# Kernel tuning notes

Measured on AMD Instinct MI355X. Metric: run time of the kernel, lower is better.

Reference implementation:

```python
import jax, jax.numpy as jnp
import numpy as np

N = 100000   # nodes
E = 1600000  # edges (no self loops; module adds them)
D = 128      # in_dim == out_dim
BN_EPS = 1e-5
NORM_EPS = 1e-12


def setup_inputs() -> dict:
    key = jax.random.key(0)
    ks = jax.random.split(key, 9)
    x = jax.random.normal(ks[0], (N, D), jnp.float32)
    src = jax.random.randint(ks[1], (E,), 0, N, dtype=jnp.int32)
    dst = jax.random.randint(ks[2], (E,), 0, N, dtype=jnp.int32)
    dst = jnp.where(dst == src, (dst + 1) % N, dst)  # no pre-existing self loops
    edge_index = jnp.stack([src, dst], axis=0)
    edge_w = jax.random.uniform(ks[3], (E, 2), jnp.float32)
    # MySAGEConv.linear: Linear(2*D -> D) since concat=True
    W_lin = jax.random.normal(ks[4], (2 * D, D), jnp.float32) * (1.0 / np.sqrt(2 * D))
    b_lin = jnp.zeros((D,), jnp.float32)
    # BatchNorm1d(D)
    gamma = jnp.ones((D,), jnp.float32)
    beta = jnp.zeros((D,), jnp.float32)
    # PositionEmbedding(2, D): Linear(2->D//2, no bias), ReLU, Linear(D//2->D, no bias)
    pos_w1 = jax.random.normal(ks[5], (2, D // 2), jnp.float32) * 0.1
    pos_w2 = jax.random.normal(ks[6], (D // 2, D), jnp.float32) * 0.1
    return {"x": x, "edge_index": edge_index, "edge_w": edge_w,
            "W_lin": W_lin, "b_lin": b_lin, "gamma": gamma, "beta": beta,
            "pos_w1": pos_w1, "pos_w2": pos_w2}


def reference(x, edge_index, edge_w, W_lin, b_lin, gamma, beta, pos_w1, pos_w2):
    src, dst = edge_index[0], edge_index[1]
    # Position embedding is computed by the block but DISCARDED inside MySAGEConv.forward,
    # because add_remaining_self_loops(edge_index, None, 1, N) overwrites edge_weight with None.
    _pe = jnp.maximum(edge_w @ pos_w1, 0.0) @ pos_w2  # [E, D], unused (faithful to bug)
    # add_remaining_self_loops: append a self loop for every node
    loops = jnp.arange(N, dtype=src.dtype)
    src_f = jnp.concatenate([src, loops])
    dst_f = jnp.concatenate([dst, loops])
    # message = x_j (edge_weight is None); aggr = 'mean' scatter over destinations
    msg = x[src_f]                                           # [E+N, D] gather
    summed = jax.ops.segment_sum(msg, dst_f, num_segments=N)  # [N, D] scatter-add
    cnt = jax.ops.segment_sum(jnp.ones((E + N, 1), x.dtype), dst_f, num_segments=N)
    aggr = summed / cnt                                      # every node has >=1 (self loop)
    # update: concat + linear + L2 normalize
    h = jnp.concatenate([x, aggr], axis=-1) @ W_lin + b_lin   # [N, D]
    h = h / jnp.maximum(jnp.linalg.norm(h, axis=-1, keepdims=True), NORM_EPS)
    # BatchNorm1d (training-mode batch stats, biased variance)
    mu = jnp.mean(h, axis=0)
    var = jnp.var(h, axis=0)
    h = (h - mu) * jax.lax.rsqrt(var + BN_EPS) * gamma + beta
    # residual (in_dim == out_dim) + ReLU
    return jnp.maximum(h + x, 0.0)
```

## Files before the change

kernel.cpp:

```cpp
#include <hip/hip_runtime.h>
#include <hip/hip_bf16.h>

typedef __attribute__((ext_vector_type(4))) float f32x4;
typedef __attribute__((ext_vector_type(8))) short short8;
typedef unsigned short u16;
typedef unsigned long long u64;

#define NSLICE 64
#define LDSN 12544

static __device__ __forceinline__ u16 f2bf(float f) {
    __hip_bfloat16 h = __float2bfloat16(f);
    return __builtin_bit_cast(u16, h);
}
static __device__ __forceinline__ float bf2f(u16 u) {
    unsigned int w = ((unsigned int)u) << 16;
    return __builtin_bit_cast(float, w);
}

__global__ void k_pre(const float* __restrict__ x, u16* __restrict__ xb, int total8,
                      const int* __restrict__ dst, int* __restrict__ part,
                      int E, int chunk, int n, int cvtBlocks, int sl4) {
    __shared__ int lh[LDSN];
    int tid = threadIdx.x;
    if ((int)blockIdx.x < cvtBlocks) {
        const float4* x4 = (const float4*)x;
        int stride = cvtBlocks * 256;
        for (int i = blockIdx.x * 256 + tid; i < total8; i += stride) {
            float4 a = x4[i * 2], b = x4[i * 2 + 1];
            union { u16 u[8]; short8 v; } o;
            o.u[0] = f2bf(a.x); o.u[1] = f2bf(a.y); o.u[2] = f2bf(a.z); o.u[3] = f2bf(a.w);
            o.u[4] = f2bf(b.x); o.u[5] = f2bf(b.y); o.u[6] = f2bf(b.z); o.u[7] = f2bf(b.w);
            *(short8*)(xb + (size_t)i * 8) = o.v;
        }
    } else {
        int b = blockIdx.x - cvtBlocks;
        int g = b & 7;
        int s = b >> 3;
        int lo = g * chunk;
        int hi = min(lo + chunk, n);
        int cnt = hi - lo;
        for (int i = tid; i < cnt; i += 256) lh[i] = 0;
        __syncthreads();
        int E4 = E >> 2;
        const int4* d4 = (const int4*)dst;
        int i40 = s * sl4, i41 = min(i40 + sl4, E4);
        for (int i = i40 + tid; i < i41; i += 256) {
            int4 v = d4[i];
            if (v.x >= lo && v.x < hi) atomicAdd(&lh[v.x - lo], 1);
            if (v.y >= lo && v.y < hi) atomicAdd(&lh[v.y - lo], 1);
            if (v.z >= lo && v.z < hi) atomicAdd(&lh[v.z - lo], 1);
            if (v.w >= lo && v.w < hi) atomicAdd(&lh[v.w - lo], 1);
        }
        if (s == NSLICE - 1) {
            for (int e = E4 * 4 + tid; e < E; e += 256) {
                int d = dst[e];
                if (d >= lo && d < hi) atomicAdd(&lh[d - lo], 1);
            }
        }
        __syncthreads();
        int* pp = part + (size_t)s * n + lo;
        for (int i = tid; i < cnt; i += 256) pp[i] = lh[i];
    }
}

__global__ void k_scan_a(int* __restrict__ part, int* __restrict__ deg,
                         int* __restrict__ bsum, int n) {
    __shared__ int sm[256];
    int tid = threadIdx.x;
    int i = blockIdx.x * 256 + tid;
    int tot = 0;
    if (i < n) {
        int run = 0;
#pragma unroll
        for (int s = 0; s < NSLICE; ++s) {
            size_t idx = (size_t)s * n + i;
            int t = part[idx];
            part[idx] = run;
            run += t;
        }
        tot = run;
        deg[i] = run;
    }
    sm[tid] = tot;
    __syncthreads();
    for (int ofs = 128; ofs > 0; ofs >>= 1) {
        if (tid < ofs) sm[tid] += sm[tid + ofs];
        __syncthreads();
    }
    if (tid == 0) bsum[blockIdx.x] = sm[0];
}

__global__ void k_scan_b(const int* __restrict__ bsum, int* __restrict__ boff, int nb,
                         int* __restrict__ offN) {
    __shared__ int s[512];
    int tid = threadIdx.x;
    int v = (tid < nb) ? bsum[tid] : 0;
    s[tid] = v;
    __syncthreads();
    for (int ofs = 1; ofs < 512; ofs <<= 1) {
        int t = (tid >= ofs) ? s[tid - ofs] : 0;
        __syncthreads();
        s[tid] += t;
        __syncthreads();
    }
    if (tid < nb) boff[tid] = s[tid] - v;
    if (tid == nb - 1) offN[0] = s[tid];
}

__global__ void k_scan_c(const int* __restrict__ deg, const int* __restrict__ boff,
                         int* __restrict__ off, int n) {
    __shared__ int s[256];
    int tid = threadIdx.x;
    int i = blockIdx.x * 256 + tid;
    int v = (i < n) ? deg[i] : 0;
    s[tid] = v;
    __syncthreads();
    for (int ofs = 1; ofs < 256; ofs <<= 1) {
        int t = (tid >= ofs) ? s[tid - ofs] : 0;
        __syncthreads();
        s[tid] += t;
        __syncthreads();
    }
    int excl = s[tid] - v + boff[blockIdx.x];
    if (i < n) off[i] = excl;
}

__global__ void k_fill(const int* __restrict__ src, const int* __restrict__ dst,
                       const int* __restrict__ off, const int* __restrict__ pre,
                       int* __restrict__ csr, int E, int chunk, int n, int sl4) {
    __shared__ int lcnt[LDSN];
    int tid = threadIdx.x;
    int g = blockIdx.x & 7;
    int s = blockIdx.x >> 3;
    int lo = g * chunk;
    int hi = min(lo + chunk, n);
    int cnt = hi - lo;
    for (int i = tid; i < cnt; i += 256) lcnt[i] = 0;
    __syncthreads();
    int E4 = E >> 2;
    const int4* d4 = (const int4*)dst;
    const int4* s4 = (const int4*)src;
    const int* prs = pre + (size_t)s * n;
    int i40 = s * sl4, i41 = min(i40 + sl4, E4);
    for (int i = i40 + tid; i < i41; i += 256) {
        int4 v = d4[i];
        int4 u = s4[i];
        if (v.x >= lo && v.x < hi) {
            int p = off[v.x] + prs[v.x] + atomicAdd(&lcnt[v.x - lo], 1);
            csr[p] = u.x;
        }
        if (v.y >= lo && v.y < hi) {
            int p = off[v.y] + prs[v.y] + atomicAdd(&lcnt[v.y - lo], 1);
            csr[p] = u.y;
        }
        if (v.z >= lo && v.z < hi) {
            int p = off[v.z] + prs[v.z] + atomicAdd(&lcnt[v.z - lo], 1);
            csr[p] = u.z;
        }
        if (v.w >= lo && v.w < hi) {
            int p = off[v.w] + prs[v.w] + atomicAdd(&lcnt[v.w - lo], 1);
            csr[p] = u.w;
        }
    }
    if (s == NSLICE - 1) {
        for (int e = E4 * 4 + tid; e < E; e += 256) {
            int d = dst[e];
            if (d >= lo && d < hi) {
                int p = off[d] + prs[d] + atomicAdd(&lcnt[d - lo], 1);
                csr[p] = src[e];
            }
        }
    }
}

__global__ void k_aggr(const u16* __restrict__ xb, const int* __restrict__ off,
                       const int* __restrict__ csr, u16* __restrict__ aggr, int n) {
    int node = (blockIdx.x * blockDim.x + threadIdx.x) >> 6;
    if (node >= n) return;
    int lane = threadIdx.x & 63;
    int c = lane & 15;
    int j = lane >> 4;
    const short8* x8 = (const short8*)xb;
    int s0 = off[node], s1 = off[node + 1];
    float acc[8] = {0.f, 0.f, 0.f, 0.f, 0.f, 0.f, 0.f, 0.f};
    int e = s0;
    for (; e + 16 <= s1; e += 16) {
        int r0 = csr[e + j], r1 = csr[e + j + 4], r2 = csr[e + j + 8], r3 = csr[e + j + 12];
        short8 v0 = x8[(size_t)r0 * 16 + c];
        short8 v1 = x8[(size_t)r1 * 16 + c];
        short8 v2 = x8[(size_t)r2 * 16 + c];
        short8 v3 = x8[(size_t)r3 * 16 + c];
#pragma unroll
        for (int i = 0; i < 8; ++i)
            acc[i] += (bf2f((u16)v0[i]) + bf2f((u16)v1[i])) +
                      (bf2f((u16)v2[i]) + bf2f((u16)v3[i]));
    }
    for (int r = e + j; r < s1; r += 4) {
        short8 v = x8[(size_t)csr[r] * 16 + c];
#pragma unroll
        for (int i = 0; i < 8; ++i) acc[i] += bf2f((u16)v[i]);
    }
#pragma unroll
    for (int i = 0; i < 8; ++i) {
        acc[i] += __shfl_xor(acc[i], 16, 64);
        acc[i] += __shfl_xor(acc[i], 32, 64);
    }
    if (j == 0) {
        short8 sv = x8[(size_t)node * 16 + c];
        float inv = 1.0f / (float)(s1 - s0 + 1);
        short8 o;
#pragma unroll
        for (int i = 0; i < 8; ++i)
            o[i] = (short)f2bf((acc[i] + bf2f((u16)sv[i])) * inv);
        *(short8*)(aggr + (size_t)node * 128 + c * 8) = o;
    }
}

__global__ __launch_bounds__(512, 2) void k_linear(
    const float* __restrict__ x, const u16* __restrict__ aggr,
    const float* __restrict__ W, const float* __restrict__ b_lin,
    u16* __restrict__ hout ,
    float* __restrict__ ssp, float* __restrict__ bnsum, float* __restrict__ bnsq,
    int n, int ntiles, int npad) {
    int tid = threadIdx.x;
    int wave = tid >> 6, l = tid & 63, lr = l & 15, lg = l >> 4;
    int pair = wave >> 1, hf = wave & 1;

    short8 breg[4][8];
#pragma unroll
    for (int ct2 = 0; ct2 < 4; ++ct2) {
        int col = hf * 64 + ct2 * 16 + lr;
#pragma unroll
        for (int kk = 0; kk < 8; ++kk) {
            int k0 = kk * 32 + 4 * lg;
            const float* wp = W + (size_t)k0 * 128 + col;
            short8 b;
#pragma unroll
            for (int j = 0; j < 4; ++j) {
                b[j]     = (short)f2bf(wp[j * 128]);
                b[4 + j] = (short)f2bf(wp[(16 + j) * 128]);
            }
            breg[ct2][kk] = b;
        }
    }

    int stride4 = gridDim.x * 4;

    for (int base = blockIdx.x * 4; base < ntiles; base += stride4) {
        int tile = base + pair;
        bool active = tile < ntiles;
        int rowA = tile * 16 + lr;
        bool rv = active && rowA < n;

        float4 xa[4], xc[4];
        ushort4 ua[4], ub[4];
#pragma unroll
        for (int kk = 0; kk < 4; ++kk) {
            int k1 = kk * 32 + 4 * lg;
            xa[kk] = rv ? *(const float4*)(x + (size_t)rowA * 128 + k1)
                        : make_float4(0.f, 0.f, 0.f, 0.f);
            xc[kk] = rv ? *(const float4*)(x + (size_t)rowA * 128 + k1 + 16)
                        : make_float4(0.f, 0.f, 0.f, 0.f);
        }
#pragma unroll
        for (int kk = 0; kk < 4; ++kk) {
            const u16* ap = aggr + (size_t)rowA * 128 + kk * 32 + 4 * lg;
            ua[kk] = rv ? *(const ushort4*)ap : make_ushort4(0, 0, 0, 0);
            ub[kk] = rv ? *(const ushort4*)(ap + 16) : make_ushort4(0, 0, 0, 0);
        }

        short8 av[8];
#pragma unroll
        for (int kk = 0; kk < 4; ++kk) {
            av[kk][0] = (short)f2bf(xa[kk].x); av[kk][1] = (short)f2bf(xa[kk].y);
            av[kk][2] = (short)f2bf(xa[kk].z); av[kk][3] = (short)f2bf(xa[kk].w);
            av[kk][4] = (short)f2bf(xc[kk].x); av[kk][5] = (short)f2bf(xc[kk].y);
            av[kk][6] = (short)f2bf(xc[kk].z); av[kk][7] = (short)f2bf(xc[kk].w);
            av[kk + 4][0] = (short)ua[kk].x; av[kk + 4][1] = (short)ua[kk].y;
            av[kk + 4][2] = (short)ua[kk].z; av[kk + 4][3] = (short)ua[kk].w;
            av[kk + 4][4] = (short)ub[kk].x; av[kk + 4][5] = (short)ub[kk].y;
            av[kk + 4][6] = (short)ub[kk].z; av[kk + 4][7] = (short)ub[kk].w;
        }

        f32x4 acc[4];
#pragma unroll
        for (int ct2 = 0; ct2 < 4; ++ct2) acc[ct2] = (f32x4){0.f, 0.f, 0.f, 0.f};
#pragma unroll
        for (int kk = 0; kk < 8; ++kk)
#pragma unroll
            for (int ct2 = 0; ct2 < 4; ++ct2)
                acc[ct2] = __builtin_amdgcn_mfma_f32_16x16x32_bf16(av[kk], breg[ct2][kk],
                                                                   acc[ct2], 0, 0, 0);

        float ss[4] = {0.f, 0.f, 0.f, 0.f};
#pragma unroll
        for (int ct2 = 0; ct2 < 4; ++ct2) {
            float bl = b_lin[hf * 64 + ct2 * 16 + lr];
#pragma unroll
            for (int q = 0; q < 4; ++q) {
                acc[ct2][q] += bl;
                ss[q] += acc[ct2][q] * acc[ct2][q];
            }
        }
#pragma unroll
        for (int m = 1; m < 16; m <<= 1) {
#pragma unroll
            for (int q = 0; q < 4; ++q) ss[q] += __shfl_xor(ss[q], m, 64);
        }
        if (active) {
            int rq0 = tile * 16 + 4 * lg;
            if (lr == 0)
                *(float4*)&ssp[hf * npad + rq0] = make_float4(ss[0], ss[1], ss[2], ss[3]);
            u16* hp = hout + (size_t)tile * 4096 + 2048;
#pragma unroll
            for (int ct2 = 0; ct2 < 4; ++ct2) {
                ushort4 o;
                o.x = f2bf(acc[ct2][0]); o.y = f2bf(acc[ct2][1]);
                o.z = f2bf(acc[ct2][2]); o.w = f2bf(acc[ct2][3]);
                *(ushort4*)(hp + (hf * 4 + ct2) * 256 + l * 4) = o;
            }
        }
    }

    __syncthreads();

    float s1a[4] = {0, 0, 0, 0};
    float s2a[4] = {0, 0, 0, 0};
    for (int base = blockIdx.x * 4; base < ntiles; base += stride4) {
        int tile = base + pair;
        if (tile >= ntiles) continue;
        int rq0 = tile * 16 + 4 * lg;
        float rn[4];
#pragma unroll
        for (int q = 0; q < 4; ++q) {
            float s2 = ssp[rq0 + q] + ssp[npad + rq0 + q];
            rn[q] = 1.0f / fmaxf(sqrtf(s2), 1e-12f);
        }
        const u16* hp = hout + (size_t)tile * 4096 + 2048;
#pragma unroll
        for (int ct2 = 0; ct2 < 4; ++ct2) {
            ushort4 hv = *(const ushort4*)(hp + (hf * 4 + ct2) * 256 + l * 4);
            float p1 = 0.f, p2 = 0.f;
            float h0 = bf2f(hv.x) * rn[0], h1 = bf2f(hv.y) * rn[1];
            float h2 = bf2f(hv.z) * rn[2], h3 = bf2f(hv.w) * rn[3];
            if (rq0 + 0 < n) { p1 += h0; p2 += h0 * h0; }
            if (rq0 + 1 < n) { p1 += h1; p2 += h1 * h1; }
            if (rq0 + 2 < n) { p1 += h2; p2 += h2 * h2; }
            if (rq0 + 3 < n) { p1 += h3; p2 += h3 * h3; }
            s1a[ct2] += p1; s2a[ct2] += p2;
        }
    }

#pragma unroll
    for (int ct2 = 0; ct2 < 4; ++ct2) {
        float v1 = s1a[ct2], v2 = s2a[ct2];
        v1 += __shfl_xor(v1, 16, 64); v1 += __shfl_xor(v1, 32, 64);
        v2 += __shfl_xor(v2, 16, 64); v2 += __shfl_xor(v2, 32, 64);
        if (lg == 0) {
            atomicAdd(&bnsum[hf * 64 + ct2 * 16 + lr], v1);
            atomicAdd(&bnsq[hf * 64 + ct2 * 16 + lr], v2);
        }
    }
}

__global__ __launch_bounds__(512) void k_final(
    const float* __restrict__ ssp, const float* __restrict__ x,
    const float* __restrict__ bnsum, const float* __restrict__ bnsq,
    const float* __restrict__ gamma, const float* __restrict__ beta,
    float* __restrict__ out, float invN, int n, int npad) {
    __shared__ float cf[256];
    __shared__ float ot[16 * 132];
    int tid = threadIdx.x;
    int tile = blockIdx.x;
    if (tid < 128) {
        float mu = bnsum[tid] * invN;
        float var = bnsq[tid] * invN - mu * mu;
        float a = gamma[tid] * rsqrtf(var + 1e-5f);
        cf[tid] = a;
        cf[128 + tid] = beta[tid] - mu * a;
    }
    __syncthreads();

    {
        const u16* hp = (const u16*)out + (size_t)tile * 4096 + 2048;
        int ct = tid >> 6, l = tid & 63;
        ushort4 hv = *(const ushort4*)(hp + ct * 256 + l * 4);
        int col = ct * 16 + (l & 15);
        float a = cf[col], b = cf[128 + col];
        int rl0 = 4 * (l >> 4);
        int rq0 = tile * 16 + rl0;
        float rn0 = 1.0f / fmaxf(sqrtf(ssp[rq0 + 0] + ssp[npad + rq0 + 0]), 1e-12f);
        float rn1 = 1.0f / fmaxf(sqrtf(ssp[rq0 + 1] + ssp[npad + rq0 + 1]), 1e-12f);
        float rn2 = 1.0f / fmaxf(sqrtf(ssp[rq0 + 2] + ssp[npad + rq0 + 2]), 1e-12f);
        float rn3 = 1.0f / fmaxf(sqrtf(ssp[rq0 + 3] + ssp[npad + rq0 + 3]), 1e-12f);
        ot[(rl0 + 0) * 132 + col] = bf2f(hv.x) * rn0 * a + b;
        ot[(rl0 + 1) * 132 + col] = bf2f(hv.y) * rn1 * a + b;
        ot[(rl0 + 2) * 132 + col] = bf2f(hv.z) * rn2 * a + b;
        ot[(rl0 + 3) * 132 + col] = bf2f(hv.w) * rn3 * a + b;
    }
    __syncthreads();

    {
        int rl = tid >> 5, c4 = tid & 31;
        int row = tile * 16 + rl;
        if (row < n) {
            float4 xv = *(const float4*)(x + (size_t)row * 128 + c4 * 4);
            const float* op = &ot[rl * 132 + c4 * 4];
            float4 o;
            o.x = fmaxf(op[0] + xv.x, 0.f);
            o.y = fmaxf(op[1] + xv.y, 0.f);
            o.z = fmaxf(op[2] + xv.z, 0.f);
            o.w = fmaxf(op[3] + xv.w, 0.f);
            *(float4*)(out + (size_t)row * 128 + c4 * 4) = o;
        }
    }
}

extern "C" void kernel_launch(void* const* d_in, const int* in_sizes, int n_in,
                              void* d_out, int out_size, void* d_ws, size_t ws_size,
                              hipStream_t stream) {
    const float* x     = (const float*)d_in[0];
    const int*   ei    = (const int*)d_in[1];
    const float* W     = (const float*)d_in[3];
    const float* b_lin = (const float*)d_in[4];
    const float* gamma = (const float*)d_in[5];
    const float* beta  = (const float*)d_in[6];
    int N = in_sizes[0] / 128;
    int E = in_sizes[1] / 2;
    const int* src = ei;
    const int* dst = ei + E;

    int ntiles = (N + 15) / 16;
    int npad = ntiles * 16;

    char* p = (char*)d_ws;
    auto alloc = [&](size_t bytes) { char* r = p; p += (bytes + 255) & ~(size_t)255; return r; };
    int*   deg   = (int*)alloc((size_t)N * 4);
    float* bnsum = (float*)alloc(128 * 4);
    float* bnsq  = (float*)alloc(128 * 4);
    size_t zoff  = (char*)bnsum - (char*)d_ws;
    int*   off   = (int*)alloc((size_t)(N + 1) * 4);
    int*   csr   = (int*)alloc((size_t)E * 4);
    int*   bsum  = (int*)alloc(512 * 4);
    int*   boff  = (int*)alloc(512 * 4);
    float* ssp   = (float*)alloc((size_t)npad * 2 * 4);
    u16*   aggr  = (u16*)alloc((size_t)N * 128 * 2);

    int* part = (int*)aggr;

    u16* xbf = (u16*)d_out;

    hipMemsetAsync((char*)d_ws + zoff, 0, 256 * 4, stream);

    int chunk = (N + 7) / 8;
    int E4 = E >> 2;
    int sl4 = (E4 + NSLICE - 1) / NSLICE;
    const int CVTB = 768;

    k_pre<<<CVTB + 8 * NSLICE, 256, 0, stream>>>(x, xbf, N * 16, dst, part,
                                                 E, chunk, N, CVTB, sl4);
    int nb = (N + 255) / 256;
    k_scan_a<<<nb, 256, 0, stream>>>(part, deg, bsum, N);
    k_scan_b<<<1, 512, 0, stream>>>(bsum, boff, nb, off + N);
    k_scan_c<<<nb, 256, 0, stream>>>(deg, boff, off, N);
    k_fill<<<8 * NSLICE, 256, 0, stream>>>(src, dst, off, part, csr, E, chunk, N, sl4);
    k_aggr<<<(int)(((size_t)N * 64 + 255) / 256), 256, 0, stream>>>(xbf, off, csr, aggr, N);
    k_linear<<<512, 512, 0, stream>>>(x, aggr, W, b_lin, (u16*)d_out, ssp,
                                      bnsum, bnsq, N, ntiles, npad);
    k_final<<<ntiles, 512, 0, stream>>>(ssp, x, bnsum, bnsq, gamma, beta,
                                        (float*)d_out, 1.0f / (float)N, N, npad);
}
```

Baseline: 272.7 us.

## Fuse neighbor mean aggregation into linear kernel via swizzled LDS tile

Folds the CSR gather/mean aggregation into the MFMA linear kernel. Each pair of waves aggregates 16 nodes into a swizzled shared-memory tile, which then feeds the B half of the A operand directly. The x operand is now read from the bf16 copy instead of fp32, and h fragments go to a separate workspace buffer. This removes the aggr write/read round trip and one launch. In exchange, each node is gathered by only 8 lanes with serial edge iteration, block-wide syncs are added per tile, and the grid is halved, which may reduce latency hiding for the irregular gathers.

```diff
diff --git a/kernel.cpp b/kernel.cpp
--- a/kernel.cpp
+++ b/kernel.cpp
@@ -174,55 +174,14 @@
     }
 }
 
-__global__ void k_aggr(const u16* __restrict__ xb, const int* __restrict__ off,
-                       const int* __restrict__ csr, u16* __restrict__ aggr, int n) {
-    int node = (blockIdx.x * blockDim.x + threadIdx.x) >> 6;
-    if (node >= n) return;
-    int lane = threadIdx.x & 63;
-    int c = lane & 15;
-    int j = lane >> 4;
-    const short8* x8 = (const short8*)xb;
-    int s0 = off[node], s1 = off[node + 1];
-    float acc[8] = {0.f, 0.f, 0.f, 0.f, 0.f, 0.f, 0.f, 0.f};
-    int e = s0;
-    for (; e + 16 <= s1; e += 16) {
-        int r0 = csr[e + j], r1 = csr[e + j + 4], r2 = csr[e + j + 8], r3 = csr[e + j + 12];
-        short8 v0 = x8[(size_t)r0 * 16 + c];
-        short8 v1 = x8[(size_t)r1 * 16 + c];
-        short8 v2 = x8[(size_t)r2 * 16 + c];
-        short8 v3 = x8[(size_t)r3 * 16 + c];
-#pragma unroll
-        for (int i = 0; i < 8; ++i)
-            acc[i] += (bf2f((u16)v0[i]) + bf2f((u16)v1[i])) +
-                      (bf2f((u16)v2[i]) + bf2f((u16)v3[i]));
-    }
-    for (int r = e + j; r < s1; r += 4) {
-        short8 v = x8[(size_t)csr[r] * 16 + c];
-#pragma unroll
-        for (int i = 0; i < 8; ++i) acc[i] += bf2f((u16)v[i]);
-    }
-#pragma unroll
-    for (int i = 0; i < 8; ++i) {
-        acc[i] += __shfl_xor(acc[i], 16, 64);
-        acc[i] += __shfl_xor(acc[i], 32, 64);
-    }
-    if (j == 0) {
-        short8 sv = x8[(size_t)node * 16 + c];
-        float inv = 1.0f / (float)(s1 - s0 + 1);
-        short8 o;
-#pragma unroll
-        for (int i = 0; i < 8; ++i)
-            o[i] = (short)f2bf((acc[i] + bf2f((u16)sv[i])) * inv);
-        *(short8*)(aggr + (size_t)node * 128 + c * 8) = o;
-    }
-}
-
-__global__ __launch_bounds__(512, 2) void k_linear(
-    const float* __restrict__ x, const u16* __restrict__ aggr,
+__global__ __launch_bounds__(512, 2) void k_al(
+    const u16* __restrict__ xb, const int* __restrict__ off,
+    const int* __restrict__ csr,
     const float* __restrict__ W, const float* __restrict__ b_lin,
-    u16* __restrict__ hout ,
-    float* __restrict__ ssp, float* __restrict__ bnsum, float* __restrict__ bnsq,
+    u16* __restrict__ hfrag, float* __restrict__ ssp,
+    float* __restrict__ bnsum, float* __restrict__ bnsq,
     int n, int ntiles, int npad) {
+    __shared__ u16 AT[4][16][128];
     int tid = threadIdx.x;
     int wave = tid >> 6, l = tid & 63, lr = l & 15, lg = l >> 4;
     int pair = wave >> 1, hf = wave & 1;
@@ -245,42 +204,98 @@
         }
     }
 
+    const short8* x8 = (const short8*)xb;
     int stride4 = gridDim.x * 4;
 
     for (int base = blockIdx.x * 4; base < ntiles; base += stride4) {
         int tile = base + pair;
         bool active = tile < ntiles;
+
+        {
+            int nl = hf * 8 + (l >> 3);
+            int lane8 = l & 7;
+            int node = tile * 16 + nl;
+            bool nv = active && node < n;
+            float acc[16];
+#pragma unroll
+            for (int i = 0; i < 16; ++i) acc[i] = 0.f;
+            int s0 = 0, s1 = 0;
+            if (nv) { s0 = off[node]; s1 = off[node + 1]; }
+            int e = s0;
+            for (; e + 2 <= s1; e += 2) {
+                int r0 = csr[e], r1 = csr[e + 1];
+                short8 a0 = x8[(size_t)r0 * 16 + lane8 * 2];
+                short8 a1 = x8[(size_t)r0 * 16 + lane8 * 2 + 1];
+                short8 c0 = x8[(size_t)r1 * 16 + lane8 * 2];
+                short8 c1 = x8[(size_t)r1 * 16 + lane8 * 2 + 1];
+#pragma unroll
+                for (int i = 0; i < 8; ++i) {
+                    acc[i]     += bf2f((u16)a0[i]) + bf2f((u16)c0[i]);
+                    acc[8 + i] += bf2f((u16)a1[i]) + bf2f((u16)c1[i]);
+                }
+            }
+            if (e < s1) {
+                int r0 = csr[e];
+                short8 a0 = x8[(size_t)r0 * 16 + lane8 * 2];
+                short8 a1 = x8[(size_t)r0 * 16 + lane8 * 2 + 1];
+#pragma unroll
+                for (int i = 0; i < 8; ++i) {
+                    acc[i]     += bf2f((u16)a0[i]);
+                    acc[8 + i] += bf2f((u16)a1[i]);
+                }
+            }
+            float inv = 0.f;
+            if (nv) {
+                short8 sv0 = x8[(size_t)node * 16 + lane8 * 2];
+                short8 sv1 = x8[(size_t)node * 16 + lane8 * 2 + 1];
+#pragma unroll
+                for (int i = 0; i < 8; ++i) {
+                    acc[i]     += bf2f((u16)sv0[i]);
+                    acc[8 + i] += bf2f((u16)sv1[i]);
+                }
+                inv = 1.0f / (float)(s1 - s0 + 1);
+            }
+            if (active) {
+                int swz = (nl & 7) << 4;
+                char* bp = (char*)&AT[pair][0][0] + nl * 256;
+                short8 o0, o1;
+#pragma unroll
+                for (int i = 0; i < 8; ++i) {
+                    o0[i] = (short)f2bf(acc[i] * inv);
+                    o1[i] = (short)f2bf(acc[8 + i] * inv);
+                }
+                *(short8*)(bp + ((lane8 * 32) ^ swz)) = o0;
+                *(short8*)(bp + ((lane8 * 32 + 16) ^ swz)) = o1;
+            }
+        }
+        __syncthreads();
+
         int rowA = tile * 16 + lr;
         bool rv = active && rowA < n;
-
-        float4 xa[4], xc[4];
-        ushort4 ua[4], ub[4];
+        ushort4 xba[4], xbb[4];
 #pragma unroll
         for (int kk = 0; kk < 4; ++kk) {
-            int k1 = kk * 32 + 4 * lg;
-            xa[kk] = rv ? *(const float4*)(x + (size_t)rowA * 128 + k1)
-                        : make_float4(0.f, 0.f, 0.f, 0.f);
-            xc[kk] = rv ? *(const float4*)(x + (size_t)rowA * 128 + k1 + 16)
-                        : make_float4(0.f, 0.f, 0.f, 0.f);
-        }
-#pragma unroll
-        for (int kk = 0; kk < 4; ++kk) {
-            const u16* ap = aggr + (size_t)rowA * 128 + kk * 32 + 4 * lg;
-            ua[kk] = rv ? *(const ushort4*)ap : make_ushort4(0, 0, 0, 0);
-            ub[kk] = rv ? *(const ushort4*)(ap + 16) : make_ushort4(0, 0, 0, 0);
-        }
-
+            const u16* xp = xb + (size_t)rowA * 128 + kk * 32 + 4 * lg;
+            xba[kk] = rv ? *(const ushort4*)xp : make_ushort4(0, 0, 0, 0);
+            xbb[kk] = rv ? *(const ushort4*)(xp + 16) : make_ushort4(0, 0, 0, 0);
+        }
         short8 av[8];
-#pragma unroll
-        for (int kk = 0; kk < 4; ++kk) {
-            av[kk][0] = (short)f2bf(xa[kk].x); av[kk][1] = (short)f2bf(xa[kk].y);
-            av[kk][2] = (short)f2bf(xa[kk].z); av[kk][3] = (short)f2bf(xa[kk].w);
-            av[kk][4] = (short)f2bf(xc[kk].x); av[kk][5] = (short)f2bf(xc[kk].y);
-            av[kk][6] = (short)f2bf(xc[kk].z); av[kk][7] = (short)f2bf(xc[kk].w);
-            av[kk + 4][0] = (short)ua[kk].x; av[kk + 4][1] = (short)ua[kk].y;
-            av[kk + 4][2] = (short)ua[kk].z; av[kk + 4][3] = (short)ua[kk].w;
-            av[kk + 4][4] = (short)ub[kk].x; av[kk + 4][5] = (short)ub[kk].y;
-            av[kk + 4][6] = (short)ub[kk].z; av[kk + 4][7] = (short)ub[kk].w;
+        {
+            const char* rp = (const char*)&AT[pair][0][0] + lr * 256;
+            int sw = (lr & 7) << 4;
+#pragma unroll
+            for (int kk = 0; kk < 4; ++kk) {
+                av[kk][0] = (short)xba[kk].x; av[kk][1] = (short)xba[kk].y;
+                av[kk][2] = (short)xba[kk].z; av[kk][3] = (short)xba[kk].w;
+                av[kk][4] = (short)xbb[kk].x; av[kk][5] = (short)xbb[kk].y;
+                av[kk][6] = (short)xbb[kk].z; av[kk][7] = (short)xbb[kk].w;
+                int kb = kk * 64 + 8 * lg;
+                u64 lo = *(const u64*)(rp + (kb ^ sw));
+                u64 hi = *(const u64*)(rp + ((kb + 32) ^ sw));
+                union { u64 q[2]; short8 v; } bu;
+                bu.q[0] = lo; bu.q[1] = hi;
+                av[kk + 4] = bu.v;
+            }
         }
 
         f32x4 acc[4];
@@ -312,7 +327,7 @@
             int rq0 = tile * 16 + 4 * lg;
             if (lr == 0)
                 *(float4*)&ssp[hf * npad + rq0] = make_float4(ss[0], ss[1], ss[2], ss[3]);
-            u16* hp = hout + (size_t)tile * 4096 + 2048;
+            u16* hp = hfrag + (size_t)tile * 2048;
 #pragma unroll
             for (int ct2 = 0; ct2 < 4; ++ct2) {
                 ushort4 o;
@@ -321,9 +336,8 @@
                 *(ushort4*)(hp + (hf * 4 + ct2) * 256 + l * 4) = o;
             }
         }
-    }
-
-    __syncthreads();
+        __syncthreads();
+    }
 
     float s1a[4] = {0, 0, 0, 0};
     float s2a[4] = {0, 0, 0, 0};
@@ -337,7 +351,7 @@
             float s2 = ssp[rq0 + q] + ssp[npad + rq0 + q];
             rn[q] = 1.0f / fmaxf(sqrtf(s2), 1e-12f);
         }
-        const u16* hp = hout + (size_t)tile * 4096 + 2048;
+        const u16* hp = hfrag + (size_t)tile * 2048;
 #pragma unroll
         for (int ct2 = 0; ct2 < 4; ++ct2) {
             ushort4 hv = *(const ushort4*)(hp + (hf * 4 + ct2) * 256 + l * 4);
@@ -365,6 +379,7 @@
 }
 
 __global__ __launch_bounds__(512) void k_final(
+    const u16* __restrict__ hfrag,
     const float* __restrict__ ssp, const float* __restrict__ x,
     const float* __restrict__ bnsum, const float* __restrict__ bnsq,
     const float* __restrict__ gamma, const float* __restrict__ beta,
@@ -383,7 +398,7 @@
     __syncthreads();
 
     {
-        const u16* hp = (const u16*)out + (size_t)tile * 4096 + 2048;
+        const u16* hp = hfrag + (size_t)tile * 2048;
         int ct = tid >> 6, l = tid & 63;
         ushort4 hv = *(const ushort4*)(hp + ct * 256 + l * 4);
         int col = ct * 16 + (l & 15);
@@ -445,9 +460,9 @@
     int*   bsum  = (int*)alloc(512 * 4);
     int*   boff  = (int*)alloc(512 * 4);
     float* ssp   = (float*)alloc((size_t)npad * 2 * 4);
-    u16*   aggr  = (u16*)alloc((size_t)N * 128 * 2);
-
-    int* part = (int*)aggr;
+    u16*   hreg  = (u16*)alloc((size_t)npad * 128 * 2);
+
+    int* part = (int*)hreg;
 
     u16* xbf = (u16*)d_out;
 
@@ -465,9 +480,8 @@
     k_scan_b<<<1, 512, 0, stream>>>(bsum, boff, nb, off + N);
     k_scan_c<<<nb, 256, 0, stream>>>(deg, boff, off, N);
     k_fill<<<8 * NSLICE, 256, 0, stream>>>(src, dst, off, part, csr, E, chunk, N, sl4);
-    k_aggr<<<(int)(((size_t)N * 64 + 255) / 256), 256, 0, stream>>>(xbf, off, csr, aggr, N);
-    k_linear<<<512, 512, 0, stream>>>(x, aggr, W, b_lin, (u16*)d_out, ssp,
-                                      bnsum, bnsq, N, ntiles, npad);
-    k_final<<<ntiles, 512, 0, stream>>>(ssp, x, bnsum, bnsq, gamma, beta,
+    k_al<<<256, 512, 0, stream>>>(xbf, off, csr, W, b_lin, hreg, ssp,
+                                  bnsum, bnsq, N, ntiles, npad);
+    k_final<<<ntiles, 512, 0, stream>>>(hreg, ssp, x, bnsum, bnsq, gamma, beta,
                                         (float*)d_out, 1.0f / (float)N, N, npad);
 }
```

Result: faster. 262.9 us (-3.6%).
